# Performance work log

Measured on AMD Instinct MI355X. Metric: run time of the kernel, lower is better.

The kernel has to match this reference:

```python
import jax, jax.numpy as jnp
import numpy as np

B, S, H, NH = 2, 2048, 2048, 16
DH = H // NH


def setup_inputs() -> dict:
    key = jax.random.key(0)
    ks = jax.random.split(key, 9)
    scale = 1.0 / np.sqrt(H)
    inp = {
        "hidden_state": jax.random.normal(ks[0], (B, S, H), dtype=jnp.float32),
        "Wq": jax.random.normal(ks[1], (H, H), dtype=jnp.float32) * scale,
        "bq": jnp.zeros((H,), dtype=jnp.float32),
        "Wk": jax.random.normal(ks[2], (H, H), dtype=jnp.float32) * scale,
        "bk": jnp.zeros((H,), dtype=jnp.float32),
        "Wv": jax.random.normal(ks[3], (H, H), dtype=jnp.float32) * scale,
        "bv": jnp.zeros((H,), dtype=jnp.float32),
        "Wo": jax.random.normal(ks[4], (H, H), dtype=jnp.float32) * scale,
        "bo": jnp.zeros((H,), dtype=jnp.float32),
    }
    # additive causal mask: 0 on/below diagonal, large negative above
    neg = jnp.float32(-1e9)
    tri = jnp.tril(jnp.ones((S, S), dtype=bool))
    inp["causal_mask"] = jnp.where(tri, 0.0, neg)[None, None, :, :]
    return inp


def reference(hidden_state, Wq, bq, Wk, bk, Wv, bv, Wo, bo, causal_mask):
    def split_heads(x):  # [B,S,H] -> [B,NH,S,DH]
        return x.reshape(B, S, NH, DH).transpose(0, 2, 1, 3)

    q = split_heads(hidden_state @ Wq + bq)
    k = split_heads(hidden_state @ Wk + bk)
    v = split_heads(hidden_state @ Wv + bv)

    scores = jnp.einsum("bhqd,bhkd->bhqk", q, k) / jnp.sqrt(jnp.float32(DH))
    scores = scores + causal_mask
    probs = jax.nn.softmax(scores, axis=-1)
    out = jnp.einsum("bhqk,bhkd->bhqd", probs, v)  # [B,NH,S,DH]
    out = out.transpose(0, 2, 1, 3).reshape(B, S, H)
    return out @ Wo + bo
```

## Files before the change

### kernel.cpp

```cpp
#include <hip/hip_runtime.h>
#include <cstdint>

typedef __attribute__((ext_vector_type(4))) float f32x4;
typedef __attribute__((ext_vector_type(16))) float f32x16;
typedef __attribute__((ext_vector_type(8))) __bf16 bf16x8;
typedef __attribute__((ext_vector_type(4))) unsigned short u16x4;
typedef __attribute__((ext_vector_type(2))) unsigned int u32x2;
typedef __attribute__((ext_vector_type(4))) float fvec4;

#define DEV __device__ __forceinline__
#define MFMA16(a, b, c) __builtin_amdgcn_mfma_f32_16x16x32_bf16((a), (b), (c), 0, 0, 0)
#define MFMA32(a, b, c) __builtin_amdgcn_mfma_f32_32x32x16_bf16((a), (b), (c), 0, 0, 0)

DEV unsigned short f2bf(float f) {
  union { float f; uint32_t u; } c; c.f = f;
  uint32_t u = c.u;
  return (unsigned short)((u + 0x7FFFu + ((u >> 16) & 1u)) >> 16);
}

DEV unsigned int pack2(float lo, float hi) {
  union { float f; uint32_t u; } a, b;
  a.f = lo; b.f = hi;
  return __builtin_amdgcn_perm(b.u + 0x8000u, a.u + 0x8000u, 0x07060302u);
}

DEV void gll16(const void* g, void* l) {
  __builtin_amdgcn_global_load_lds(
      (const __attribute__((address_space(1))) void*)(uintptr_t)g,
      (__attribute__((address_space(3))) void*)(uint32_t)(uintptr_t)l,
      16, 0, 0);
}

__global__ void cvt_bf16(const float* __restrict__ src, unsigned short* __restrict__ dst) {
  int i = (blockIdx.x * 256 + threadIdx.x) * 4;
  fvec4 v = *(const fvec4*)(src + i);
  u16x4 o;
  o[0] = f2bf(v[0]); o[1] = f2bf(v[1]); o[2] = f2bf(v[2]); o[3] = f2bf(v[3]);
  *(u16x4*)(dst + i) = o;
}

__global__ void transpose_cvt4(const float* __restrict__ W0, const float* __restrict__ W1,
                               const float* __restrict__ W2, const float* __restrict__ W3,
                               unsigned short* __restrict__ Dqkv, unsigned short* __restrict__ Do) {
  __shared__ float t[32][33];
  const float* W = blockIdx.z == 0 ? W0 : blockIdx.z == 1 ? W1 : blockIdx.z == 2 ? W2 : W3;
  unsigned short* WT = blockIdx.z < 3 ? Dqkv + (size_t)blockIdx.z * 2048 * 2048 : Do;
  int n0 = blockIdx.x * 32, k0 = blockIdx.y * 32;
  int x = threadIdx.x, y = threadIdx.y;
  #pragma unroll
  for (int i = 0; i < 32; i += 8)
    t[y + i][x] = W[(size_t)(k0 + y + i) * 2048 + n0 + x];
  __syncthreads();
  #pragma unroll
  for (int i = 0; i < 32; i += 8)
    WT[(size_t)(n0 + y + i) * 2048 + k0 + x] = f2bf(t[x][y + i]);
}

constexpr float QSC = 0.08838834764831845f * 1.4426950408889634f;

template <int MODE>
__global__ __launch_bounds__(256, 2) void gemm128(
    const unsigned short* __restrict__ A,
    const unsigned short* __restrict__ Bt,
    const float* __restrict__ b0, const float* __restrict__ b1,
    const float* __restrict__ b2,
    void* __restrict__ o0, void* __restrict__ o1, void* __restrict__ o2) {
  __shared__ unsigned short As[128 * 64];
  __shared__ unsigned short Bs[128 * 64];
  const int id = blockIdx.x;
  const int m0 = (((id & 7) << 2) | ((id >> 3) & 3)) * 128;
  const int n0 = (id >> 5) * 128;
  const int tid = threadIdx.x;
  const int wave = tid >> 6, lid = tid & 63;
  const int l16 = lid & 15, lq = lid >> 4;
  const int wm = (wave >> 1) * 64, wn = (wave & 1) * 64;

  const int srow = lid >> 3;
  const int sgrp = (lid & 7) ^ srow;

  f32x4 acc[4][4] = {};

  for (int k0 = 0; k0 < 2048; k0 += 64) {
    #pragma unroll
    for (int i = 0; i < 4; ++i) {
      const int t = wave * 4 + i;
      const int r = t * 8 + srow;
      gll16(A + (size_t)(m0 + r) * 2048 + k0 + sgrp * 8, (char*)As + t * 1024 + lid * 16);
      gll16(Bt + (size_t)(n0 + r) * 2048 + k0 + sgrp * 8, (char*)Bs + t * 1024 + lid * 16);
    }
    __syncthreads();
    #pragma unroll
    for (int kk = 0; kk < 2; ++kk) {
      const int G = kk * 4 + lq;
      bf16x8 af[4], bfr[4];
      #pragma unroll
      for (int i = 0; i < 4; ++i)
        af[i] = *(const bf16x8*)(As + (wm + i * 16 + l16) * 64 + ((G ^ (l16 & 7)) << 3));
      #pragma unroll
      for (int j = 0; j < 4; ++j)
        bfr[j] = *(const bf16x8*)(Bs + (wn + j * 16 + l16) * 64 + ((G ^ (l16 & 7)) << 3));
      #pragma unroll
      for (int i = 0; i < 4; ++i)
        #pragma unroll
        for (int j = 0; j < 4; ++j)
          acc[i][j] = MFMA16(af[i], bfr[j], acc[i][j]);
    }
    __syncthreads();
  }

  #pragma unroll
  for (int j = 0; j < 4; ++j) {
    const int c = n0 + wn + j * 16 + l16;
    const float bv = b0[c];
    #pragma unroll
    for (int i = 0; i < 4; ++i)
      #pragma unroll
      for (int r = 0; r < 4; ++r) {
        const int row = m0 + wm + i * 16 + lq * 4 + r;
        ((float*)o0)[(size_t)row * 2048 + c] = acc[i][j][r] + bv;
      }
  }
}

__global__ __launch_bounds__(512, 2) void gemmqkv(
    const unsigned short* __restrict__ A,
    const unsigned short* __restrict__ Bt,
    const float* __restrict__ b0, const float* __restrict__ b1,
    const float* __restrict__ b2,
    unsigned short* __restrict__ oQ, unsigned short* __restrict__ oK,
    unsigned short* __restrict__ oV) {
  __shared__ unsigned short Als[2 * 128 * 64];
  __shared__ unsigned short Bls[2 * 256 * 64];

  const int id = blockIdx.x;
  const int xcd = id & 7, loc = id >> 3;
  const int mt = loc & 31, ntl = loc >> 5;
  const int nt = xcd * 3 + ntl;
  const int m0 = mt << 7, n0 = nt << 8;

  const int tid = threadIdx.x;
  const int wave = tid >> 6, lid = tid & 63;
  const int l16 = lid & 15, lq = lid >> 4;
  const int wr = wave >> 2, wc = wave & 3;
  const int srow = tid >> 3;
  const int g8 = ((tid & 7) ^ (srow & 7)) * 8;

  f32x4 acc[4][4] = {};
  bf16x8 aq[2][2], bq[4][2];

#define STA_(c, kt) do { \
    _Pragma("unroll") for (int u = 0; u < 2; ++u) \
      gll16(A + (size_t)(m0 + u * 64 + srow) * 2048 + ((kt) << 6) + g8, \
            (char*)Als + (c) * 16384 + u * 8192 + tid * 16); \
  } while (0)

#define STB_(c, kt) do { \
    _Pragma("unroll") for (int u = 0; u < 4; ++u) \
      gll16(Bt + (size_t)(n0 + u * 64 + srow) * 2048 + ((kt) << 6) + g8, \
            (char*)Bls + (c) * 32768 + u * 8192 + tid * 16); \
  } while (0)

#define RDA_(c, h) do { \
    _Pragma("unroll") for (int m = 0; m < 2; ++m) { \
      const int row = wr * 64 + ((h) * 2 + m) * 16 + l16; \
      _Pragma("unroll") for (int kk = 0; kk < 2; ++kk) \
        aq[m][kk] = *(const bf16x8*)(Als + (c) * 8192 + row * 64 + \
                                     (((kk * 4 + lq) ^ (row & 7)) << 3)); \
    } } while (0)

#define RDB_(c) do { \
    _Pragma("unroll") for (int n = 0; n < 4; ++n) { \
      const int bg = wc * 64 + n * 16 + l16; \
      _Pragma("unroll") for (int kk = 0; kk < 2; ++kk) \
        bq[n][kk] = *(const bf16x8*)(Bls + (c) * 16384 + bg * 64 + \
                                     (((kk * 4 + lq) ^ (bg & 7)) << 3)); \
    } } while (0)

#define MM_(h) do { \
    _Pragma("unroll") for (int m = 0; m < 2; ++m) \
      _Pragma("unroll") for (int n = 0; n < 4; ++n) \
        _Pragma("unroll") for (int kk = 0; kk < 2; ++kk) \
          acc[(h) * 2 + m][n] = MFMA16(aq[m][kk], bq[n][kk], acc[(h) * 2 + m][n]); \
  } while (0)

#define SB_ __builtin_amdgcn_sched_barrier(0)
#define BAR_ __builtin_amdgcn_s_barrier()
#define LGKM_ asm volatile("s_waitcnt lgkmcnt(0)" ::: "memory")
#define VM4_ asm volatile("s_waitcnt vmcnt(4)" ::: "memory")

  STB_(0, 0); STA_(0, 0); STB_(1, 1);
  VM4_;
  BAR_;

  #pragma unroll 1
  for (int i = 0; i < 16; ++i) {
    const int t1 = 2 * i + 1;
    const int t2 = (2 * i + 2 < 32) ? 2 * i + 2 : 31;
    const int t3 = (2 * i + 3 < 32) ? 2 * i + 3 : 31;
    RDA_(0, 0); RDB_(0); STA_(1, t1);
    SB_; BAR_; LGKM_; SB_;
    __builtin_amdgcn_s_setprio(1); MM_(0); __builtin_amdgcn_s_setprio(0);
    SB_; BAR_;
    RDA_(0, 1); STB_(0, t2);
    SB_; BAR_; LGKM_; SB_;
    __builtin_amdgcn_s_setprio(1); MM_(1); __builtin_amdgcn_s_setprio(0);
    SB_; VM4_; BAR_;
    RDA_(1, 0); RDB_(1); STA_(0, t2);
    SB_; BAR_; LGKM_; SB_;
    __builtin_amdgcn_s_setprio(1); MM_(0); __builtin_amdgcn_s_setprio(0);
    SB_; BAR_;
    RDA_(1, 1); STB_(1, t3);
    SB_; BAR_; LGKM_; SB_;
    __builtin_amdgcn_s_setprio(1); MM_(1); __builtin_amdgcn_s_setprio(0);
    SB_; VM4_; BAR_;
  }
  asm volatile("s_waitcnt vmcnt(0)" ::: "memory");

  const int which = n0 >> 11;
  const float* bp = which == 0 ? b0 : which == 1 ? b1 : b2;
  #pragma unroll
  for (int n = 0; n < 4; ++n) {
    const int hd = (n0 & 2047) + wc * 64 + n * 16 + l16;
    const int h = hd >> 7, d = hd & 127;
    const float bv = bp[hd];
    if (which == 2) {
      #pragma unroll
      for (int m = 0; m < 4; ++m) {
        const int row0 = m0 + wr * 64 + m * 16 + lq * 4;
        const int bb = row0 >> 11, s0 = row0 & 2047;
        u16x4 pv;
        #pragma unroll
        for (int r = 0; r < 4; ++r) pv[r] = f2bf(acc[m][n][r] + bv);
        *(u16x4*)(oV + ((size_t)((bb * 16 + h) * 128 + d)) * 2048 + s0) = pv;
      }
    } else {
      const float sc = which == 0 ? QSC : 1.0f;
      unsigned short* op = which == 0 ? oQ : oK;
      #pragma unroll
      for (int m = 0; m < 4; ++m)
        #pragma unroll
        for (int r = 0; r < 4; ++r) {
          const int row = m0 + wr * 64 + m * 16 + lq * 4 + r;
          const int bb = row >> 11, s = row & 2047;
          op[(size_t)((bb * 16 + h) * 2048 + s) * 128 + d] = f2bf((acc[m][n][r] + bv) * sc);
        }
    }
  }
#undef STA_
#undef STB_
#undef RDA_
#undef RDB_
#undef MM_
#undef SB_
#undef BAR_
#undef LGKM_
#undef VM4_
}

__global__ __launch_bounds__(256, 2) void attn(
    const unsigned short* __restrict__ Q,
    const unsigned short* __restrict__ K,
    const unsigned short* __restrict__ Vt,
    unsigned short* __restrict__ ctx) {
  __shared__ unsigned short Ks[64 * 128];
  __shared__ unsigned short Vts[128 * 64];
  __shared__ unsigned short Ps[4 * 32 * 64];

  const int bh = blockIdx.y;
  const int jq = (bh < 16) ? (15 - (int)blockIdx.x) : (int)blockIdx.x;
  const int q0 = jq * 128;
  const int b = bh >> 4, h = bh & 15;
  const unsigned short* Qh = Q + (size_t)bh * 2048 * 128;
  const unsigned short* Kh = K + (size_t)bh * 2048 * 128;
  const unsigned short* Vth = Vt + (size_t)bh * 128 * 2048;

  const int tid = threadIdx.x;
  const int wave = tid >> 6, lid = tid & 63;
  const int l32 = lid & 31, half = lid >> 5;
  const int qrow = q0 + wave * 32 + l32;
  unsigned short* Pw = Ps + wave * 2048 + l32 * 64;
  const int qsw = l32 & 7;

  bf16x8 qf[8];
  #pragma unroll
  for (int ds = 0; ds < 8; ++ds)
    qf[ds] = *(const bf16x8*)(Qh + (size_t)qrow * 128 + ds * 16 + half * 8);

  float m_i = -1e30f, l_i = 0.f;
  f32x16 acc[4] = {};

  const int ntiles = 2 * jq + 2;
  for (int jt = 0; jt < ntiles; ++jt) {
    const int k0 = jt * 64;
    #pragma unroll
    for (int ii = 0; ii < 4; ++ii) {
      const int t = wave * 4 + ii;
      const int r = t * 4 + (lid >> 4);
      const int g = (lid & 15) ^ (r & 15);
      gll16(Kh + (size_t)(k0 + r) * 128 + g * 8, (char*)Ks + t * 1024 + lid * 16);
    }
    #pragma unroll
    for (int ii = 0; ii < 4; ++ii) {
      const int t = wave * 4 + ii;
      const int d = t * 8 + (lid >> 3);
      const int g = (lid & 7) ^ (d & 7);
      gll16(Vth + (size_t)d * 2048 + k0 + g * 8, (char*)Vts + t * 1024 + lid * 16);
    }
    __syncthreads();

    f32x16 sacc[2] = {};
    #pragma unroll
    for (int ds = 0; ds < 8; ++ds) {
      #pragma unroll
      for (int mb = 0; mb < 2; ++mb) {
        const int kr = mb * 32 + l32;
        bf16x8 af = *(const bf16x8*)(Ks + kr * 128 + (((ds * 2 + half) ^ (kr & 15)) << 3));
        sacc[mb] = MFMA32(af, qf[ds], sacc[mb]);
      }
    }

    if (jt >= 2 * jq) {
      #pragma unroll
      for (int mb = 0; mb < 2; ++mb)
        #pragma unroll
        for (int i = 0; i < 16; ++i) {
          const int kg = k0 + mb * 32 + (i & 3) + 8 * (i >> 2) + 4 * half;
          if (kg > qrow) sacc[mb][i] = -1e30f;
        }
    }

    float tmax = -1e30f;
    #pragma unroll
    for (int mb = 0; mb < 2; ++mb)
      #pragma unroll
      for (int i = 0; i < 16; ++i) tmax = fmaxf(tmax, sacc[mb][i]);
    tmax = fmaxf(tmax, __shfl_xor(tmax, 32));

    const float mnew = fmaxf(m_i, tmax);
    const float alpha = exp2f(m_i - mnew);
    m_i = mnew;

    float ps = 0.f;
    #pragma unroll
    for (int mb = 0; mb < 2; ++mb) {
      #pragma unroll
      for (int i = 0; i < 16; ++i) {
        sacc[mb][i] = exp2f(sacc[mb][i] - mnew);
        ps += sacc[mb][i];
      }
      #pragma unroll
      for (int u = 0; u < 4; ++u) {
        u32x2 w;
        w[0] = pack2(sacc[mb][4 * u], sacc[mb][4 * u + 1]);
        w[1] = pack2(sacc[mb][4 * u + 2], sacc[mb][4 * u + 3]);
        *(u32x2*)(Pw + (((u + mb * 4) ^ qsw) << 3) + half * 4) = w;
      }
    }
    ps += __shfl_xor(ps, 32);
    l_i = l_i * alpha + ps;
    #pragma unroll
    for (int db = 0; db < 4; ++db)
      #pragma unroll
      for (int i = 0; i < 16; ++i) acc[db][i] *= alpha;

    #pragma unroll
    for (int ks = 0; ks < 4; ++ks) {
      bf16x8 pf = *(const bf16x8*)(Pw + (((ks * 2 + half) ^ qsw) << 3));
      #pragma unroll
      for (int db = 0; db < 4; ++db) {
        const int d = db * 32 + l32;
        bf16x8 vf = *(const bf16x8*)(Vts + d * 64 + (((ks * 2 + half) ^ (d & 7)) << 3));
        acc[db] = MFMA32(vf, pf, acc[db]);
      }
    }
    __syncthreads();
  }

  const float inv = 1.f / l_i;
  const size_t base = ((size_t)(b * 2048 + qrow)) * 2048 + h * 128;
  #pragma unroll
  for (int db = 0; db < 4; ++db) {
    #pragma unroll
    for (int u = 0; u < 4; ++u) {
      u32x2 w;
      w[0] = pack2(acc[db][4 * u] * inv, acc[db][4 * u + 1] * inv);
      w[1] = pack2(acc[db][4 * u + 2] * inv, acc[db][4 * u + 3] * inv);
      *(u32x2*)(ctx + base + db * 32 + 8 * u + 4 * half) = w;
    }
  }
}

extern "C" void kernel_launch(void* const* d_in, const int* in_sizes, int n_in,
                              void* d_out, int out_size, void* d_ws, size_t ws_size,
                              hipStream_t stream) {
  const float* hs = (const float*)d_in[0];
  const float* Wq = (const float*)d_in[1];
  const float* bq = (const float*)d_in[2];
  const float* Wk = (const float*)d_in[3];
  const float* bk = (const float*)d_in[4];
  const float* Wv = (const float*)d_in[5];
  const float* bv = (const float*)d_in[6];
  const float* Wo = (const float*)d_in[7];
  const float* bo = (const float*)d_in[8];
  float* out = (float*)d_out;

  char* ws = (char*)d_ws;
  unsigned short* hsb   = (unsigned short*)(ws);
  unsigned short* wqkvt = (unsigned short*)(ws + (16 << 20));
  unsigned short* wot   = (unsigned short*)(ws + (40 << 20));
  unsigned short* Qb    = (unsigned short*)(ws + (48 << 20));
  unsigned short* Kb    = (unsigned short*)(ws + (64 << 20));
  unsigned short* Vtb   = (unsigned short*)(ws + (80 << 20));
  unsigned short* ctx   = (unsigned short*)(ws + (96 << 20));

  cvt_bf16<<<dim3(8192), dim3(256), 0, stream>>>(hs, hsb);
  transpose_cvt4<<<dim3(64, 64, 4), dim3(32, 8), 0, stream>>>(Wq, Wk, Wv, Wo, wqkvt, wot);

  gemmqkv<<<dim3(768), dim3(512), 0, stream>>>(hsb, wqkvt, bq, bk, bv, Qb, Kb, Vtb);
  attn<<<dim3(16, 32), 256, 0, stream>>>(Qb, Kb, Vtb, ctx);
  gemm128<0><<<dim3(512), 256, 0, stream>>>(ctx, wot, bo, nullptr, nullptr,
                                            (void*)out, nullptr, nullptr);
}
```

Before: 389.0 us.

## Retile QKV GEMM to 256x192 blocks with simplified per-k-step pipeline

Changes the fused QKV projection GEMM from 128x256 tiles (768 blocks) to 256x192 tiles (512 blocks), so each wave computes 128x48 and all A/B fragments for a k-step are loaded at once. The main loop becomes one iteration per 64-wide k-step, with the next tile's global loads issued between the two MFMA halves and fewer barriers per step. The aim is more arithmetic per byte of LDS and global traffic and less synchronisation. In exchange it uses more registers per thread (8x2 A fragments, 8x3 accumulators), 80 KB of LDS per block, and gives only 512 blocks, which may hurt occupancy or tail balance. Output tiles can now cross the Q/K/V boundaries, so the bias and destination are chosen per column.

```diff
diff --git a/kernel.cpp b/kernel.cpp
--- a/kernel.cpp
+++ b/kernel.cpp
@@ -129,14 +129,14 @@
     const float* __restrict__ b2,
     unsigned short* __restrict__ oQ, unsigned short* __restrict__ oK,
     unsigned short* __restrict__ oV) {
-  __shared__ unsigned short Als[2 * 128 * 64];
-  __shared__ unsigned short Bls[2 * 256 * 64];
+  __shared__ unsigned short Als[2 * 256 * 64];
+  __shared__ unsigned short Bls[2 * 192 * 64];
 
   const int id = blockIdx.x;
   const int xcd = id & 7, loc = id >> 3;
-  const int mt = loc & 31, ntl = loc >> 5;
-  const int nt = xcd * 3 + ntl;
-  const int m0 = mt << 7, n0 = nt << 8;
+  const int nt = xcd * 4 + (loc >> 4);
+  const int mt = loc & 15;
+  const int m0 = mt << 8, n0 = nt * 192;
 
   const int tid = threadIdx.x;
   const int wave = tid >> 6, lid = tid & 63;
@@ -145,88 +145,80 @@
   const int srow = tid >> 3;
   const int g8 = ((tid & 7) ^ (srow & 7)) * 8;
 
-  f32x4 acc[4][4] = {};
-  bf16x8 aq[2][2], bq[4][2];
+  f32x4 acc[8][3] = {};
+  bf16x8 aq[8][2], bq[3][2];
 
 #define STA_(c, kt) do { \
-    _Pragma("unroll") for (int u = 0; u < 2; ++u) \
+    _Pragma("unroll") for (int u = 0; u < 4; ++u) \
       gll16(A + (size_t)(m0 + u * 64 + srow) * 2048 + ((kt) << 6) + g8, \
-            (char*)Als + (c) * 16384 + u * 8192 + tid * 16); \
+            (char*)Als + (c) * 32768 + u * 8192 + tid * 16); \
   } while (0)
 
 #define STB_(c, kt) do { \
-    _Pragma("unroll") for (int u = 0; u < 4; ++u) \
+    _Pragma("unroll") for (int u = 0; u < 3; ++u) \
       gll16(Bt + (size_t)(n0 + u * 64 + srow) * 2048 + ((kt) << 6) + g8, \
-            (char*)Bls + (c) * 32768 + u * 8192 + tid * 16); \
+            (char*)Bls + (c) * 24576 + u * 8192 + tid * 16); \
   } while (0)
 
-#define RDA_(c, h) do { \
-    _Pragma("unroll") for (int m = 0; m < 2; ++m) { \
-      const int row = wr * 64 + ((h) * 2 + m) * 16 + l16; \
+#define RDALL_(c) do { \
+    _Pragma("unroll") for (int mf = 0; mf < 8; ++mf) { \
+      const int row = wr * 128 + mf * 16 + l16; \
       _Pragma("unroll") for (int kk = 0; kk < 2; ++kk) \
-        aq[m][kk] = *(const bf16x8*)(Als + (c) * 8192 + row * 64 + \
-                                     (((kk * 4 + lq) ^ (row & 7)) << 3)); \
-    } } while (0)
-
-#define RDB_(c) do { \
-    _Pragma("unroll") for (int n = 0; n < 4; ++n) { \
-      const int bg = wc * 64 + n * 16 + l16; \
+        aq[mf][kk] = *(const bf16x8*)(Als + (c) * 16384 + row * 64 + \
+                                      (((kk * 4 + lq) ^ (row & 7)) << 3)); \
+    } \
+    _Pragma("unroll") for (int n = 0; n < 3; ++n) { \
+      const int bg = wc * 48 + n * 16 + l16; \
       _Pragma("unroll") for (int kk = 0; kk < 2; ++kk) \
-        bq[n][kk] = *(const bf16x8*)(Bls + (c) * 16384 + bg * 64 + \
+        bq[n][kk] = *(const bf16x8*)(Bls + (c) * 12288 + bg * 64 + \
                                      (((kk * 4 + lq) ^ (bg & 7)) << 3)); \
     } } while (0)
 
 #define MM_(h) do { \
-    _Pragma("unroll") for (int m = 0; m < 2; ++m) \
-      _Pragma("unroll") for (int n = 0; n < 4; ++n) \
+    _Pragma("unroll") for (int m = 0; m < 4; ++m) \
+      _Pragma("unroll") for (int n = 0; n < 3; ++n) \
         _Pragma("unroll") for (int kk = 0; kk < 2; ++kk) \
-          acc[(h) * 2 + m][n] = MFMA16(aq[m][kk], bq[n][kk], acc[(h) * 2 + m][n]); \
+          acc[(h) * 4 + m][n] = MFMA16(aq[(h) * 4 + m][kk], bq[n][kk], acc[(h) * 4 + m][n]); \
   } while (0)
 
 #define SB_ __builtin_amdgcn_sched_barrier(0)
 #define BAR_ __builtin_amdgcn_s_barrier()
 #define LGKM_ asm volatile("s_waitcnt lgkmcnt(0)" ::: "memory")
-#define VM4_ asm volatile("s_waitcnt vmcnt(4)" ::: "memory")
-
-  STB_(0, 0); STA_(0, 0); STB_(1, 1);
-  VM4_;
+#define VM7_ asm volatile("s_waitcnt vmcnt(7)" ::: "memory")
+
+  STA_(0, 0); STB_(0, 0);
+  STA_(1, 1); STB_(1, 1);
+  VM7_;
   BAR_;
 
   #pragma unroll 1
-  for (int i = 0; i < 16; ++i) {
-    const int t1 = 2 * i + 1;
-    const int t2 = (2 * i + 2 < 32) ? 2 * i + 2 : 31;
-    const int t3 = (2 * i + 3 < 32) ? 2 * i + 3 : 31;
-    RDA_(0, 0); RDB_(0); STA_(1, t1);
-    SB_; BAR_; LGKM_; SB_;
+  for (int t = 0; t < 32; ++t) {
+    const int c = t & 1;
+    const int tn = (t + 2 < 32) ? t + 2 : 31;
+    RDALL_(c);
+    SB_; LGKM_; SB_;
     __builtin_amdgcn_s_setprio(1); MM_(0); __builtin_amdgcn_s_setprio(0);
     SB_; BAR_;
-    RDA_(0, 1); STB_(0, t2);
-    SB_; BAR_; LGKM_; SB_;
+    STA_(c, tn); STB_(c, tn);
+    SB_;
     __builtin_amdgcn_s_setprio(1); MM_(1); __builtin_amdgcn_s_setprio(0);
-    SB_; VM4_; BAR_;
-    RDA_(1, 0); RDB_(1); STA_(0, t2);
-    SB_; BAR_; LGKM_; SB_;
-    __builtin_amdgcn_s_setprio(1); MM_(0); __builtin_amdgcn_s_setprio(0);
-    SB_; BAR_;
-    RDA_(1, 1); STB_(1, t3);
-    SB_; BAR_; LGKM_; SB_;
-    __builtin_amdgcn_s_setprio(1); MM_(1); __builtin_amdgcn_s_setprio(0);
-    SB_; VM4_; BAR_;
+    SB_; VM7_;
+    BAR_;
   }
   asm volatile("s_waitcnt vmcnt(0)" ::: "memory");
 
-  const int which = n0 >> 11;
-  const float* bp = which == 0 ? b0 : which == 1 ? b1 : b2;
-  #pragma unroll
-  for (int n = 0; n < 4; ++n) {
-    const int hd = (n0 & 2047) + wc * 64 + n * 16 + l16;
+  #pragma unroll
+  for (int n = 0; n < 3; ++n) {
+    const int cgl = n0 + wc * 48 + n * 16 + l16;
+    const int which = cgl >> 11;
+    const int hd = cgl & 2047;
     const int h = hd >> 7, d = hd & 127;
+    const float* bp = which == 0 ? b0 : which == 1 ? b1 : b2;
     const float bv = bp[hd];
     if (which == 2) {
       #pragma unroll
-      for (int m = 0; m < 4; ++m) {
-        const int row0 = m0 + wr * 64 + m * 16 + lq * 4;
+      for (int m = 0; m < 8; ++m) {
+        const int row0 = m0 + wr * 128 + m * 16 + lq * 4;
         const int bb = row0 >> 11, s0 = row0 & 2047;
         u16x4 pv;
         #pragma unroll
@@ -237,10 +229,10 @@
       const float sc = which == 0 ? QSC : 1.0f;
       unsigned short* op = which == 0 ? oQ : oK;
       #pragma unroll
-      for (int m = 0; m < 4; ++m)
+      for (int m = 0; m < 8; ++m)
         #pragma unroll
         for (int r = 0; r < 4; ++r) {
-          const int row = m0 + wr * 64 + m * 16 + lq * 4 + r;
+          const int row = m0 + wr * 128 + m * 16 + lq * 4 + r;
           const int bb = row >> 11, s = row & 2047;
           op[(size_t)((bb * 16 + h) * 2048 + s) * 128 + d] = f2bf((acc[m][n][r] + bv) * sc);
         }
@@ -248,13 +240,12 @@
   }
 #undef STA_
 #undef STB_
-#undef RDA_
-#undef RDB_
+#undef RDALL_
 #undef MM_
 #undef SB_
 #undef BAR_
 #undef LGKM_
-#undef VM4_
+#undef VM7_
 }
 
 __global__ __launch_bounds__(256, 2) void attn(
@@ -416,7 +407,7 @@
   cvt_bf16<<<dim3(8192), dim3(256), 0, stream>>>(hs, hsb);
   transpose_cvt4<<<dim3(64, 64, 4), dim3(32, 8), 0, stream>>>(Wq, Wk, Wv, Wo, wqkvt, wot);
 
-  gemmqkv<<<dim3(768), dim3(512), 0, stream>>>(hsb, wqkvt, bq, bk, bv, Qb, Kb, Vtb);
+  gemmqkv<<<dim3(512), dim3(512), 0, stream>>>(hsb, wqkvt, bq, bk, bv, Qb, Kb, Vtb);
   attn<<<dim3(16, 32), 256, 0, stream>>>(Qb, Kb, Vtb, ctx);
   gemm128<0><<<dim3(512), 256, 0, stream>>>(ctx, wot, bo, nullptr, nullptr,
                                             (void*)out, nullptr, nullptr);
```

New measurement: 388.6 us. Within noise of the previous version (-0.1%).
